# Kernel optimization log

Measured on AMD Instinct MI355X. Metric: run time of the kernel, lower is better.

## Reference

```python
import jax, jax.numpy as jnp
import numpy as np

B, H1, H2, D, C = 4096, 32, 32, 32, 64


def setup_inputs() -> dict:
    key = jax.random.key(0)
    k1, k2, k3 = jax.random.split(key, 3)
    x = jax.random.normal(k1, (B, H1, D), dtype=jnp.float32)
    y = jax.random.normal(k2, (B, H2, D), dtype=jnp.float32)
    # glorot-uniform-ish kernel of shape (compress_dim, H1, H2)
    limit = float(np.sqrt(6.0 / (H1 + H2)))
    kernel = jax.random.uniform(k3, (C, H1, H2), dtype=jnp.float32,
                                minval=-limit, maxval=limit)
    return {"x": x, "y": y, "kernel": kernel}


def reference(x, y, kernel):
    # Original math: outer[b,i,j,d] = x[b,i,d]*y[b,j,d];
    # output_mat[b,c,d] = sum_{i,j} outer[b,i,j,d] * kernel[c,i,j]
    # Expressed as a fused bilinear contraction (avoids the [B,H1,H2,D] tensor):
    # first fold kernel into y per compress channel, then contract with x.
    t = jnp.einsum('cij,bjd->bcid', kernel, y)       # [B,C,H1,D]
    output_mat = jnp.einsum('bid,bcid->bcd', x, t)   # [B,C,D]
    final_output = jnp.sum(output_mat, axis=-1)      # [B,C]
    return (output_mat, final_output)
```

## Files before the change

kernel.cpp:

```cpp
#include <hip/hip_runtime.h>
#include <hip/hip_bf16.h>


typedef __attribute__((ext_vector_type(8))) short short8;
typedef __attribute__((ext_vector_type(4))) float f32x4;

__device__ __forceinline__ unsigned short f2bf_rne(float f) {
    union { float f; unsigned u; } w; w.f = f;
    return (unsigned short)((w.u + 0x7FFFu + ((w.u >> 16) & 1u)) >> 16);
}

__global__ __launch_bounds__(256) void kswz_kernel(const float* __restrict__ kern,
                                                   short* __restrict__ kswz) {
    int f    = blockIdx.x * 256 + threadIdx.x;
    int ntl  = f & 1;
    int lane = (f >> 1) & 63;
    int nth  = (f >> 7) & 1;
    int s    = f >> 8;
    int c    = (nth * 2 + ntl) * 16 + (lane & 15);
    int jb   = (lane >> 4) * 8;
    const float* src = kern + c * 1024 + s * 32 + jb;
    short8 v;
#pragma unroll
    for (int t = 0; t < 8; ++t) v[t] = (short)f2bf_rne(src[t]);
    *(short8*)(kswz + (size_t)f * 8) = v;
}

__global__ __launch_bounds__(256, 4) void cin_main(const float* __restrict__ x,
                                                   const float* __restrict__ y,
                                                   const short* __restrict__ kswz,
                                                   float* __restrict__ out_mat,
                                                   float* __restrict__ out_fin) {
    __shared__ float xs[4 * 1024];

    const int tid  = threadIdx.x;
    const int wave = tid >> 6;
    const int lane = tid & 63;
    const int quad = lane >> 4;
    const int n16  = lane & 15;
    const int b_blk = blockIdx.x * 4;
    const int bpair = wave >> 1;
    const int nth   = wave & 1;

    {
        const float4* xg = (const float4*)(x + (size_t)b_blk * 1024);
        float4* xs4 = (float4*)xs;
#pragma unroll
        for (int i = 0; i < 4; ++i) xs4[tid + 256 * i] = xg[tid + 256 * i];
    }

    const int b0 = b_blk + bpair * 2;

    float yv[4][8];
#pragma unroll
    for (int mt = 0; mt < 4; ++mt) {
        const int b = b0 + (mt >> 1);
        const int d = n16 + 16 * (mt & 1);
        const float* yp = y + (size_t)b * 1024 + (quad * 8) * 32 + d;
#pragma unroll
        for (int t = 0; t < 8; ++t) yv[mt][t] = yp[t * 32];
    }

    f32x4 acc[4][2];
#pragma unroll
    for (int mt = 0; mt < 4; ++mt)
#pragma unroll
        for (int ntl = 0; ntl < 2; ++ntl) acc[mt][ntl] = (f32x4){0.f, 0.f, 0.f, 0.f};

    const char* kb = (const char*)kswz + (size_t)(nth * 2048 + lane * 32);
    int xoff[4];
#pragma unroll
    for (int mt = 0; mt < 4; ++mt)
        xoff[mt] = (bpair * 2 + (mt >> 1)) * 1024 + n16 + 16 * (mt & 1);

    __syncthreads();

    short8 bc0 = *(const short8*)(kb);
    short8 bc1 = *(const short8*)(kb + 16);
    float xc[4];
#pragma unroll
    for (int mt = 0; mt < 4; ++mt) xc[mt] = xs[xoff[mt]];

#pragma unroll
    for (int s = 0; s < 32; ++s) {
        short8 bn0, bn1;
        float xn[4];
        if (s < 31) {
            bn0 = *(const short8*)(kb + (s + 1) * 4096);
            bn1 = *(const short8*)(kb + (s + 1) * 4096 + 16);
#pragma unroll
            for (int mt = 0; mt < 4; ++mt) xn[mt] = xs[xoff[mt] + (s + 1) * 32];
        }

#pragma unroll
        for (int mt = 0; mt < 4; ++mt) {
            union { short8 s8; __hip_bfloat162 h2[4]; } af;
            const float xv = xc[mt];
#pragma unroll
            for (int p = 0; p < 4; ++p) {
                float2 pr = make_float2(xv * yv[mt][2 * p], xv * yv[mt][2 * p + 1]);
                af.h2[p] = __float22bfloat162_rn(pr);
            }
            acc[mt][0] = __builtin_amdgcn_mfma_f32_16x16x32_bf16(af.s8, bc0, acc[mt][0], 0, 0, 0);
            acc[mt][1] = __builtin_amdgcn_mfma_f32_16x16x32_bf16(af.s8, bc1, acc[mt][1], 0, 0, 0);
        }

        bc0 = bn0; bc1 = bn1;
#pragma unroll
        for (int mt = 0; mt < 4; ++mt) xc[mt] = xn[mt];
    }

#pragma unroll
    for (int mt = 0; mt < 4; ++mt) {
        const int b = b0 + (mt >> 1);
        const int dbase = 16 * (mt & 1) + quad * 4;
#pragma unroll
        for (int ntl = 0; ntl < 2; ++ntl) {
            const int c = (nth * 2 + ntl) * 16 + n16;
            *(f32x4*)(out_mat + (size_t)b * 2048 + c * 32 + dbase) = acc[mt][ntl];
        }
    }

#pragma unroll
    for (int a = 0; a < 2; ++a) {
        const int b = b0 + a;
#pragma unroll
        for (int ntl = 0; ntl < 2; ++ntl) {
            float f = 0.f;
#pragma unroll
            for (int t = 0; t < 4; ++t) f += acc[2 * a][ntl][t] + acc[2 * a + 1][ntl][t];
            f += __shfl_xor(f, 16);
            f += __shfl_xor(f, 32);
            if (lane < 16) out_fin[(size_t)b * 64 + (nth * 2 + ntl) * 16 + n16] = f;
        }
    }
}

extern "C" void kernel_launch(void* const* d_in, const int* in_sizes, int n_in,
                              void* d_out, int out_size, void* d_ws, size_t ws_size,
                              hipStream_t stream) {
    const float* x    = (const float*)d_in[0];
    const float* y    = (const float*)d_in[1];
    const float* kern = (const float*)d_in[2];
    float* out_mat = (float*)d_out;
    float* out_fin = (float*)d_out + 4096 * 64 * 32;
    short* kswz = (short*)d_ws;

    kswz_kernel<<<32, 256, 0, stream>>>(kern, kswz);
    cin_main<<<1024, 256, 0, stream>>>(x, y, kswz, out_mat, out_fin);
}
```

Before: 109.4 us.

## Stage swizzled kernel weights through double-buffered LDS with async global-to-LDS loads

Kernel weight fragments are no longer read straight from global memory by each wave. Each block now copies 16 KB chunks into a double-buffered LDS array with global_load_lds, walking the chunks in a block-dependent rotated order, and every wave reads its B fragments from LDS. The x tile is also loaded with async direct-to-LDS copies, and the weight swizzle layout changes to match. The goal is to cut repeated per-wave global/L2 weight traffic and overlap loads with MFMA work, at the cost of more LDS (about 48 KB), lower occupancy (launch bound 3) and a __syncthreads per chunk.

```diff
diff --git a/kernel.cpp b/kernel.cpp
--- a/kernel.cpp
+++ b/kernel.cpp
@@ -12,26 +12,32 @@
 
 __global__ __launch_bounds__(256) void kswz_kernel(const float* __restrict__ kern,
                                                    short* __restrict__ kswz) {
-    int f    = blockIdx.x * 256 + threadIdx.x;
-    int ntl  = f & 1;
-    int lane = (f >> 1) & 63;
-    int nth  = (f >> 7) & 1;
-    int s    = f >> 8;
-    int c    = (nth * 2 + ntl) * 16 + (lane & 15);
+    int idx  = blockIdx.x * 256 + threadIdx.x;
+    int lane = idx & 63;
+    int nt   = (idx >> 6) & 3;
+    int s    = idx >> 8;
+    int c    = nt * 16 + (lane & 15);
     int jb   = (lane >> 4) * 8;
     const float* src = kern + c * 1024 + s * 32 + jb;
     short8 v;
 #pragma unroll
     for (int t = 0; t < 8; ++t) v[t] = (short)f2bf_rne(src[t]);
-    *(short8*)(kswz + (size_t)f * 8) = v;
+    *(short8*)(kswz + (size_t)idx * 8) = v;
 }
 
-__global__ __launch_bounds__(256, 4) void cin_main(const float* __restrict__ x,
+__device__ __forceinline__ void gld_lds16(const void* g, void* l) {
+    __builtin_amdgcn_global_load_lds(
+        (const __attribute__((address_space(1))) unsigned int*)g,
+        (__attribute__((address_space(3))) unsigned int*)l, 16, 0, 0);
+}
+
+__global__ __launch_bounds__(256, 3) void cin_main(const float* __restrict__ x,
                                                    const float* __restrict__ y,
                                                    const short* __restrict__ kswz,
                                                    float* __restrict__ out_mat,
                                                    float* __restrict__ out_fin) {
-    __shared__ float xs[4 * 1024];
+    __shared__ __align__(16) float xs[4 * 1024];
+    __shared__ __align__(16) short kb[2][8192];
 
     const int tid  = threadIdx.x;
     const int wave = tid >> 6;
@@ -43,11 +49,16 @@
     const int nth   = wave & 1;
 
     {
-        const float4* xg = (const float4*)(x + (size_t)b_blk * 1024);
-        float4* xs4 = (float4*)xs;
+        const float* xg = x + (size_t)b_blk * 1024;
 #pragma unroll
-        for (int i = 0; i < 4; ++i) xs4[tid + 256 * i] = xg[tid + 256 * i];
+        for (int r = 0; r < 4; ++r)
+            gld_lds16(xg + (r * 256 + tid) * 4, &xs[r * 1024 + wave * 256]);
     }
+    const int cq0 = blockIdx.x & 7;
+#pragma unroll
+    for (int r = 0; r < 4; ++r)
+        gld_lds16(kswz + ((size_t)cq0 * 8192 + (r * 256 + tid) * 8),
+                  &kb[0][r * 2048 + wave * 512]);
 
     const int b0 = b_blk + bpair * 2;
 
@@ -67,7 +78,7 @@
 #pragma unroll
         for (int ntl = 0; ntl < 2; ++ntl) acc[mt][ntl] = (f32x4){0.f, 0.f, 0.f, 0.f};
 
-    const char* kb = (const char*)kswz + (size_t)(nth * 2048 + lane * 32);
+    const short* kbL[2] = { &kb[0][lane * 8], &kb[1][lane * 8] };
     int xoff[4];
 #pragma unroll
     for (int mt = 0; mt < 4; ++mt)
@@ -75,39 +86,36 @@
 
     __syncthreads();
 
-    short8 bc0 = *(const short8*)(kb);
-    short8 bc1 = *(const short8*)(kb + 16);
-    float xc[4];
+    for (int p = 0; p < 8; ++p) {
+        if (p < 7) {
+            const int cn = (cq0 + p + 1) & 7;
+            short* dst = (short*)&kb[(p + 1) & 1][0];
 #pragma unroll
-    for (int mt = 0; mt < 4; ++mt) xc[mt] = xs[xoff[mt]];
-
-#pragma unroll
-    for (int s = 0; s < 32; ++s) {
-        short8 bn0, bn1;
-        float xn[4];
-        if (s < 31) {
-            bn0 = *(const short8*)(kb + (s + 1) * 4096);
-            bn1 = *(const short8*)(kb + (s + 1) * 4096 + 16);
-#pragma unroll
-            for (int mt = 0; mt < 4; ++mt) xn[mt] = xs[xoff[mt] + (s + 1) * 32];
+            for (int r = 0; r < 4; ++r)
+                gld_lds16(kswz + ((size_t)cn * 8192 + (r * 256 + tid) * 8),
+                          dst + r * 2048 + wave * 512);
         }
 
+        const short* kbase = kbL[p & 1];
+        const int sbase = ((cq0 + p) & 7) * 4;
 #pragma unroll
-        for (int mt = 0; mt < 4; ++mt) {
-            union { short8 s8; __hip_bfloat162 h2[4]; } af;
-            const float xv = xc[mt];
+        for (int k = 0; k < 4; ++k) {
+            const short8 bf0 = *(const short8*)(kbase + (k * 4 + nth * 2) * 512);
+            const short8 bf1 = *(const short8*)(kbase + (k * 4 + nth * 2 + 1) * 512);
 #pragma unroll
-            for (int p = 0; p < 4; ++p) {
-                float2 pr = make_float2(xv * yv[mt][2 * p], xv * yv[mt][2 * p + 1]);
-                af.h2[p] = __float22bfloat162_rn(pr);
+            for (int mt = 0; mt < 4; ++mt) {
+                const float xv = xs[xoff[mt] + (sbase + k) * 32];
+                union { short8 s8; __hip_bfloat162 h2[4]; } af;
+#pragma unroll
+                for (int pp = 0; pp < 4; ++pp) {
+                    float2 pr = make_float2(xv * yv[mt][2 * pp], xv * yv[mt][2 * pp + 1]);
+                    af.h2[pp] = __float22bfloat162_rn(pr);
+                }
+                acc[mt][0] = __builtin_amdgcn_mfma_f32_16x16x32_bf16(af.s8, bf0, acc[mt][0], 0, 0, 0);
+                acc[mt][1] = __builtin_amdgcn_mfma_f32_16x16x32_bf16(af.s8, bf1, acc[mt][1], 0, 0, 0);
             }
-            acc[mt][0] = __builtin_amdgcn_mfma_f32_16x16x32_bf16(af.s8, bc0, acc[mt][0], 0, 0, 0);
-            acc[mt][1] = __builtin_amdgcn_mfma_f32_16x16x32_bf16(af.s8, bc1, acc[mt][1], 0, 0, 0);
         }
-
-        bc0 = bn0; bc1 = bn1;
-#pragma unroll
-        for (int mt = 0; mt < 4; ++mt) xc[mt] = xn[mt];
+        __syncthreads();
     }
 
 #pragma unroll
```

Measured after the change: 111.9 us. 2.3% more time.
